# Kernel tuning notes

Measured on AMD Instinct MI355X. Metric: run time of the kernel, lower is better.

## Reference

```python
import jax, jax.numpy as jnp
import numpy as np

B, S, D_IN, D_K, D_OUT = 8, 2048, 1024, 64, 64

def setup_inputs() -> dict:
    key = jax.random.key(0)
    k1, k2, k3, k4 = jax.random.split(key, 4)
    sc = 1.0 / np.sqrt(D_IN)
    return {
        "X": jax.random.normal(k1, (B, S, D_IN), dtype=jnp.float32),
        "Wq": jax.random.normal(k2, (D_IN, D_K), dtype=jnp.float32) * sc,
        "Wk": jax.random.normal(k3, (D_IN, D_K), dtype=jnp.float32) * sc,
        "Wv": jax.random.normal(k4, (D_IN, D_OUT), dtype=jnp.float32) * sc,
    }

def reference(X, Wq, Wk, Wv):
    # projections (no bias)
    Q = jnp.einsum('bsd,dk->bsk', X, Wq)   # [B,S,d_k]
    K = jnp.einsum('bsd,dk->bsk', X, Wk)   # [B,S,d_k]
    V = jnp.einsum('bsd,dv->bsv', X, Wv)   # [B,S,d_out]
    d_k = Q.shape[-1]
    S_mat = jnp.einsum('bqk,bsk->bqs', Q, K) / jnp.sqrt(jnp.float32(d_k))
    # causal mask: positions j > i get -inf
    causal = jnp.tril(jnp.ones((X.shape[1], X.shape[1]), dtype=bool))
    S_mat = jnp.where(causal[None, :, :], S_mat, -jnp.inf)
    A = jax.nn.softmax(S_mat, axis=-1)
    return jnp.einsum('bqs,bsv->bqv', A, V)
```

## Files before the change

kernel.cpp:

```cpp
#include <hip/hip_runtime.h>
#include <hip/hip_bf16.h>
#include <cstdint>
#include <cstddef>

#define BATCH 8
#define SEQ   2048
#define DIN   1024

typedef float f32x4 __attribute__((ext_vector_type(4)));
typedef float f32x8 __attribute__((ext_vector_type(8)));
typedef __bf16 bf16x4 __attribute__((ext_vector_type(4)));
typedef __bf16 bf16x8 __attribute__((ext_vector_type(8)));
typedef unsigned short ushort8_t __attribute__((ext_vector_type(8)));

__device__ __forceinline__ unsigned short bfu(float f) {
  __bf16 h = (__bf16)f;
  return __builtin_bit_cast(unsigned short, h);
}

__device__ __forceinline__ bf16x8 cvt8pair(float4 a, float4 b) {
  f32x8 v;
  v[0] = a.x; v[1] = a.y; v[2] = a.z; v[3] = a.w;
  v[4] = b.x; v[5] = b.y; v[6] = b.z; v[7] = b.w;
  return __builtin_convertvector(v, bf16x8);
}

__global__ void pack_w(const float* __restrict__ Wq, const float* __restrict__ Wk,
                       const float* __restrict__ Wv, unsigned short* __restrict__ Wp) {
  const int t = blockIdx.x * blockDim.x + threadIdx.x;
  const int lane = t & 63;
  const int grp = t >> 6;
  const int ks = grp & 31;
  const int nt = grp >> 5;
  const int n = nt * 16 + (lane & 15);
  const int k0 = ks * 32 + ((lane >> 4) << 3);
  const float* W;
  int col;
  float scale = 1.0f;
  if (n < 64)       { W = Wq; col = n;       scale = 0.18033688011112042f; }
  else if (n < 128) { W = Wk; col = n - 64;  }
  else              { W = Wv; col = n - 128; }
  ushort8_t out;
#pragma unroll
  for (int j = 0; j < 8; ++j)
    out[j] = bfu(W[(size_t)(k0 + j) * 64 + col] * scale);
  reinterpret_cast<ushort8_t*>(Wp)[t] = out;
}

__global__ __launch_bounds__(256, 2) void qkv_gemm(
    const float* __restrict__ X, const unsigned short* __restrict__ Wp,
    unsigned short* __restrict__ Qb, unsigned short* __restrict__ Kf,
    unsigned short* __restrict__ Vf) {
  __shared__ ushort8_t Af[2][2048];

  const int tid = threadIdx.x;
  const int lane = tid & 63;
  const int wave = tid >> 6;
  const int l15 = lane & 15;
  const int quad = lane >> 4;
  const int m0 = blockIdx.x * 32;
  const int nt0 = wave * 3;

  const int sr = tid >> 3;
  const int sk = tid & 7;
  const float* xrow = X + (size_t)(m0 + sr) * DIN;

  const ushort8_t* wp = reinterpret_cast<const ushort8_t*>(Wp) + nt0 * 2048 + lane;
  ushort8_t breg[2][3];
#pragma unroll
  for (int p = 0; p < 2; ++p)
#pragma unroll
    for (int nt = 0; nt < 3; ++nt) breg[p][nt] = wp[p * 64 + nt * 2048];

  f32x4 acc[2][3];
#pragma unroll
  for (int mt = 0; mt < 2; ++mt)
#pragma unroll
    for (int nt = 0; nt < 3; ++nt) acc[mt][nt] = (f32x4){0.f, 0.f, 0.f, 0.f};

  auto compute_half = [&](int ksbase, const ushort8_t* A) {
    ushort8_t a0 = A[quad * 32 + l15];
    ushort8_t a1 = A[quad * 32 + 16 + l15];
    for (int ksl = 0; ksl < 16; ++ksl) {
      const int ks = ksbase + ksl;
      const int p = ks & 1;
      bf16x8 af0 = __builtin_bit_cast(bf16x8, a0);
      bf16x8 af1 = __builtin_bit_cast(bf16x8, a1);
      bf16x8 b0 = __builtin_bit_cast(bf16x8, breg[p][0]);
      bf16x8 b1 = __builtin_bit_cast(bf16x8, breg[p][1]);
      bf16x8 b2 = __builtin_bit_cast(bf16x8, breg[p][2]);
      if (ksl < 15) {
        a0 = A[((ksl + 1) * 4 + quad) * 32 + l15];
        a1 = A[((ksl + 1) * 4 + quad) * 32 + 16 + l15];
      }
      if (ks < 30) {
#pragma unroll
        for (int nt = 0; nt < 3; ++nt)
          breg[p][nt] = wp[(ks + 2) * 64 + nt * 2048];
      }
      acc[0][0] = __builtin_amdgcn_mfma_f32_16x16x32_bf16(af0, b0, acc[0][0], 0, 0, 0);
      acc[0][1] = __builtin_amdgcn_mfma_f32_16x16x32_bf16(af0, b1, acc[0][1], 0, 0, 0);
      acc[0][2] = __builtin_amdgcn_mfma_f32_16x16x32_bf16(af0, b2, acc[0][2], 0, 0, 0);
      acc[1][0] = __builtin_amdgcn_mfma_f32_16x16x32_bf16(af1, b0, acc[1][0], 0, 0, 0);
      acc[1][1] = __builtin_amdgcn_mfma_f32_16x16x32_bf16(af1, b1, acc[1][1], 0, 0, 0);
      acc[1][2] = __builtin_amdgcn_mfma_f32_16x16x32_bf16(af1, b2, acc[1][2], 0, 0, 0);
    }
  };

  float4 xbuf[16];
#pragma unroll
  for (int p = 0; p < 2; ++p) {
    const float4* src = reinterpret_cast<const float4*>(xrow + (sk + p * 8) * 32);
#pragma unroll
    for (int i = 0; i < 8; ++i) xbuf[p * 8 + i] = src[i];
  }
#pragma unroll
  for (int p = 0; p < 2; ++p) {
    const int ksl = sk + p * 8;
#pragma unroll
    for (int q = 0; q < 4; ++q)
      Af[0][(ksl * 4 + q) * 32 + sr] =
          __builtin_bit_cast(ushort8_t, cvt8pair(xbuf[p * 8 + q * 2], xbuf[p * 8 + q * 2 + 1]));
  }
  __syncthreads();

#pragma unroll
  for (int p = 0; p < 2; ++p) {
    const float4* src = reinterpret_cast<const float4*>(xrow + (16 + sk + p * 8) * 32);
#pragma unroll
    for (int i = 0; i < 8; ++i) xbuf[p * 8 + i] = src[i];
  }

  compute_half(0, Af[0]);

#pragma unroll
  for (int p = 0; p < 2; ++p) {
    const int ksl = sk + p * 8;
#pragma unroll
    for (int q = 0; q < 4; ++q)
      Af[1][(ksl * 4 + q) * 32 + sr] =
          __builtin_bit_cast(ushort8_t, cvt8pair(xbuf[p * 8 + q * 2], xbuf[p * 8 + q * 2 + 1]));
  }
  __syncthreads();

  compute_half(16, Af[1]);

#pragma unroll
  for (int mt = 0; mt < 2; ++mt) {
    const int srow = m0 + mt * 16 + quad * 4;
    const int b = srow >> 11;
    const int s = srow & 2047;
#pragma unroll
    for (int nt = 0; nt < 3; ++nt) {
      const f32x4 a = acc[mt][nt];
      const int n = (nt0 + nt) * 16 + l15;
      if (n < 64) {
#pragma unroll
        for (int r = 0; r < 4; ++r)
          Qb[(size_t)(srow + r) * 64 + n] = bfu(a[r]);
      } else if (n < 128) {
        const int dk = n - 64;
        const int dh = dk >> 5, kq = (dk >> 3) & 3, kj = dk & 7;
        const int kt = s >> 6, hh = (s >> 4) & 3;
        unsigned short* kdst = Kf + (((size_t)(b * 32 + kt) * 8 + hh * 2 + dh) << 9)
                                  + (kq * 16 + quad * 4) * 8 + kj;
#pragma unroll
        for (int r = 0; r < 4; ++r) kdst[r * 8] = bfu(a[r]);
      } else {
        const int dv = n - 128;
        const int vnt = dv >> 4, vl = dv & 15;
        const int kt = s >> 6, vc = (s >> 5) & 1, vq = (s >> 3) & 3, j0 = s & 7;
        ushort4 t4;
        t4.x = bfu(a[0]); t4.y = bfu(a[1]);
        t4.z = bfu(a[2]); t4.w = bfu(a[3]);
        *reinterpret_cast<ushort4*>(Vf + (((size_t)(b * 32 + kt) * 8 + vc * 4 + vnt) << 9)
                                       + (vq * 16 + vl) * 8 + j0) = t4;
      }
    }
  }
}

__global__ __launch_bounds__(256, 2) void flash_kernel(
    const unsigned short* __restrict__ Qb, const unsigned short* __restrict__ Kf,
    const unsigned short* __restrict__ Vf, float* __restrict__ Out) {
  __shared__ float Olds[4][2][16][68];
  __shared__ float Llds[4][2][16];
  __shared__ __attribute__((aligned(16))) unsigned short Pf[4][2][2][512];

  const int tid = threadIdx.x;
  const int lane = tid & 63;
  const int wave = tid >> 6;
  const int l15 = lane & 15;
  const int quad = lane >> 4;

  const int g = blockIdx.x;
  const int batch = g & 7;
  const int jj = (g >> 3) & 31;
  const int qb = (g < 256) ? (63 - jj) : jj;
  const int q0 = qb * 32;
  const int n64 = (q0 + 95) >> 6;

  bf16x8 qf[2][2];
#pragma unroll
  for (int mt = 0; mt < 2; ++mt) {
    const ushort8_t* qp = reinterpret_cast<const ushort8_t*>(
        Qb + (size_t)(batch * SEQ + q0 + mt * 16 + l15) * 64);
    qf[mt][0] = __builtin_bit_cast(bf16x8, qp[quad]);
    qf[mt][1] = __builtin_bit_cast(bf16x8, qp[4 + quad]);
  }

  const ushort8_t* kfb = reinterpret_cast<const ushort8_t*>(Kf)
                         + (size_t)batch * 32 * 512 + lane;
  const ushort8_t* vfb = reinterpret_cast<const ushort8_t*>(Vf)
                         + (size_t)batch * 32 * 512 + lane;

  const int pbase = l15 * 8 + (quad >> 1) * 128 + (quad & 1) * 4;

  f32x4 o[2][4];
  float lacc[2];
#pragma unroll
  for (int mt = 0; mt < 2; ++mt) {
    lacc[mt] = 0.f;
#pragma unroll
    for (int i = 0; i < 4; ++i) o[mt][i] = (f32x4){0.f, 0.f, 0.f, 0.f};
  }

  ushort8_t kbuf[8];
  if (wave < n64) {
    const ushort8_t* kp = kfb + wave * 512;
#pragma unroll
    for (int i = 0; i < 8; ++i) kbuf[i] = kp[i * 64];
  }

  for (int kt = wave; kt < n64; kt += 4) {
    const int k0 = kt * 64;
    f32x4 s[2][4];
    __builtin_amdgcn_s_setprio(1);
#pragma unroll
    for (int h = 0; h < 4; ++h) {
      bf16x8 kf0 = __builtin_bit_cast(bf16x8, kbuf[h * 2]);
      bf16x8 kf1 = __builtin_bit_cast(bf16x8, kbuf[h * 2 + 1]);
#pragma unroll
      for (int mt = 0; mt < 2; ++mt) {
        f32x4 z = (f32x4){0.f, 0.f, 0.f, 0.f};
        z = __builtin_amdgcn_mfma_f32_16x16x32_bf16(kf0, qf[mt][0], z, 0, 0, 0);
        z = __builtin_amdgcn_mfma_f32_16x16x32_bf16(kf1, qf[mt][1], z, 0, 0, 0);
        s[mt][h] = z;
      }
    }
    __builtin_amdgcn_s_setprio(0);
    {
      const int nk = (kt + 4 < n64) ? kt + 4 : n64 - 1;
      const ushort8_t* kp = kfb + nk * 512;
#pragma unroll
      for (int i = 0; i < 8; ++i) kbuf[i] = kp[i * 64];
    }
    ushort8_t vbuf[8];
    {
      const ushort8_t* vp = vfb + kt * 512;
#pragma unroll
      for (int i = 0; i < 8; ++i) vbuf[i] = vp[i * 64];
    }
    if (kt == n64 - 1) {
#pragma unroll
      for (int mt = 0; mt < 2; ++mt) {
        const int row = q0 + mt * 16 + l15;
#pragma unroll
        for (int h = 0; h < 4; ++h) {
          const int colb = k0 + h * 16 + quad * 4;
#pragma unroll
          for (int r = 0; r < 4; ++r)
            if (colb + r > row) s[mt][h][r] = -INFINITY;
        }
      }
    }
#pragma unroll
    for (int mt = 0; mt < 2; ++mt) {
#pragma unroll
      for (int h = 0; h < 4; ++h) {
        f32x4 p;
#pragma unroll
        for (int r = 0; r < 4; ++r) p[r] = __builtin_amdgcn_exp2f(s[mt][h][r]);
        lacc[mt] += (p[0] + p[1]) + (p[2] + p[3]);
        bf16x4 pk = __builtin_convertvector(p, bf16x4);
        *reinterpret_cast<unsigned long long*>(
            &Pf[wave][mt][h >> 1][pbase + ((h & 1) << 8)]) =
            __builtin_bit_cast(unsigned long long, pk);
      }
    }
#pragma unroll
    for (int c = 0; c < 2; ++c) {
      bf16x8 pfm[2];
#pragma unroll
      for (int mt = 0; mt < 2; ++mt)
        pfm[mt] = __builtin_bit_cast(bf16x8,
            reinterpret_cast<const ushort8_t*>(&Pf[wave][mt][c][0])[lane]);
      __builtin_amdgcn_s_setprio(1);
#pragma unroll
      for (int nt = 0; nt < 4; ++nt) {
        bf16x8 vf = __builtin_bit_cast(bf16x8, vbuf[c * 4 + nt]);
#pragma unroll
        for (int mt = 0; mt < 2; ++mt)
          o[mt][nt] = __builtin_amdgcn_mfma_f32_16x16x32_bf16(pfm[mt], vf, o[mt][nt], 0, 0, 0);
      }
      __builtin_amdgcn_s_setprio(0);
    }
  }

#pragma unroll
  for (int off = 16; off < 64; off <<= 1)
#pragma unroll
    for (int mt = 0; mt < 2; ++mt)
      lacc[mt] += __shfl_xor(lacc[mt], off, 64);

#pragma unroll
  for (int mt = 0; mt < 2; ++mt) {
#pragma unroll
    for (int nt = 0; nt < 4; ++nt)
#pragma unroll
      for (int r = 0; r < 4; ++r)
        Olds[wave][mt][quad * 4 + r][nt * 16 + l15] = o[mt][nt][r];
    if (quad == 0) Llds[wave][mt][l15] = lacc[mt];
  }
  __syncthreads();

  const int col = tid & 63;
  const int r0 = tid >> 6;
#pragma unroll
  for (int row = r0; row < 32; row += 4) {
    const int mt = row >> 4;
    const int rr = row & 15;
    float lstar = 0.f, accv = 0.f;
#pragma unroll
    for (int w = 0; w < 4; ++w) {
      lstar += Llds[w][mt][rr];
      accv += Olds[w][mt][rr][col];
    }
    Out[(size_t)(batch * SEQ + q0 + row) * 64 + col] = accv / lstar;
  }
}

extern "C" void kernel_launch(void* const* d_in, const int* in_sizes, int n_in,
                              void* d_out, int out_size, void* d_ws, size_t ws_size,
                              hipStream_t stream) {
  const float* X  = (const float*)d_in[0];
  const float* Wq = (const float*)d_in[1];
  const float* Wk = (const float*)d_in[2];
  const float* Wv = (const float*)d_in[3];
  float* Out = (float*)d_out;

  char* ws = (char*)d_ws;
  unsigned short* Wp = (unsigned short*)ws;
  unsigned short* Qb = (unsigned short*)(ws + (400 << 10));
  unsigned short* Kf = (unsigned short*)(ws + (400 << 10) + (2 << 20));
  unsigned short* Vf = (unsigned short*)(ws + (400 << 10) + (4 << 20));

  pack_w<<<96, 256, 0, stream>>>(Wq, Wk, Wv, Wp);
  qkv_gemm<<<512, 256, 0, stream>>>(X, Wp, Qb, Kf, Vf);
  flash_kernel<<<512, 256, 0, stream>>>(Qb, Kf, Vf, Out);
}
```

Before: 121.1 us.

## Use 64-row query tiles with 8 waves splitting KV tiles per block

The flash kernel now gives each block 64 query rows and 512 threads (8 waves), each wave handling every eighth KV tile, so each K/V tile load feeds four 16-row MMA groups instead of two. The grid halves to 256 blocks, and the reversed/paired query-block ordering used for causal load balancing is dropped. The cross-wave output reduction reuses the P scratch buffer in LDS one 16-row slice at a time, with extra barriers. This raises per-wave register pressure and leaves blocks with very uneven work because of the causal mask. Short query blocks also leave most waves idle.

```diff
diff --git a/kernel.cpp b/kernel.cpp
--- a/kernel.cpp
+++ b/kernel.cpp
@@ -180,12 +180,12 @@
   }
 }
 
-__global__ __launch_bounds__(256, 2) void flash_kernel(
+__global__ __launch_bounds__(512, 2) void flash_kernel(
     const unsigned short* __restrict__ Qb, const unsigned short* __restrict__ Kf,
     const unsigned short* __restrict__ Vf, float* __restrict__ Out) {
-  __shared__ float Olds[4][2][16][68];
-  __shared__ float Llds[4][2][16];
-  __shared__ __attribute__((aligned(16))) unsigned short Pf[4][2][2][512];
+  __shared__ __attribute__((aligned(16))) unsigned short Pf[8][4][2][512];
+  __shared__ float Llds[8][4][16];
+  float* Om = reinterpret_cast<float*>(&Pf[0][0][0][0]);
 
   const int tid = threadIdx.x;
   const int lane = tid & 63;
@@ -195,14 +195,13 @@
 
   const int g = blockIdx.x;
   const int batch = g & 7;
-  const int jj = (g >> 3) & 31;
-  const int qb = (g < 256) ? (63 - jj) : jj;
-  const int q0 = qb * 32;
-  const int n64 = (q0 + 95) >> 6;
-
-  bf16x8 qf[2][2];
-#pragma unroll
-  for (int mt = 0; mt < 2; ++mt) {
+  const int qb = g >> 3;
+  const int q0 = qb * 64;
+  const int n64 = qb + 1;
+
+  bf16x8 qf[4][2];
+#pragma unroll
+  for (int mt = 0; mt < 4; ++mt) {
     const ushort8_t* qp = reinterpret_cast<const ushort8_t*>(
         Qb + (size_t)(batch * SEQ + q0 + mt * 16 + l15) * 64);
     qf[mt][0] = __builtin_bit_cast(bf16x8, qp[quad]);
@@ -216,127 +215,127 @@
 
   const int pbase = l15 * 8 + (quad >> 1) * 128 + (quad & 1) * 4;
 
-  f32x4 o[2][4];
-  float lacc[2];
-#pragma unroll
-  for (int mt = 0; mt < 2; ++mt) {
+  f32x4 o[4][4];
+  float lacc[4];
+#pragma unroll
+  for (int mt = 0; mt < 4; ++mt) {
     lacc[mt] = 0.f;
 #pragma unroll
     for (int i = 0; i < 4; ++i) o[mt][i] = (f32x4){0.f, 0.f, 0.f, 0.f};
   }
 
-  ushort8_t kbuf[8];
+  ushort8_t kbuf[8], vbuf[8];
+
   if (wave < n64) {
-    const ushort8_t* kp = kfb + wave * 512;
-#pragma unroll
-    for (int i = 0; i < 8; ++i) kbuf[i] = kp[i * 64];
-  }
-
-  for (int kt = wave; kt < n64; kt += 4) {
-    const int k0 = kt * 64;
-    f32x4 s[2][4];
-    __builtin_amdgcn_s_setprio(1);
-#pragma unroll
-    for (int h = 0; h < 4; ++h) {
-      bf16x8 kf0 = __builtin_bit_cast(bf16x8, kbuf[h * 2]);
-      bf16x8 kf1 = __builtin_bit_cast(bf16x8, kbuf[h * 2 + 1]);
-#pragma unroll
-      for (int mt = 0; mt < 2; ++mt) {
-        f32x4 z = (f32x4){0.f, 0.f, 0.f, 0.f};
-        z = __builtin_amdgcn_mfma_f32_16x16x32_bf16(kf0, qf[mt][0], z, 0, 0, 0);
-        z = __builtin_amdgcn_mfma_f32_16x16x32_bf16(kf1, qf[mt][1], z, 0, 0, 0);
-        s[mt][h] = z;
-      }
-    }
-    __builtin_amdgcn_s_setprio(0);
     {
-      const int nk = (kt + 4 < n64) ? kt + 4 : n64 - 1;
-      const ushort8_t* kp = kfb + nk * 512;
+      const ushort8_t* kp = kfb + wave * 512;
 #pragma unroll
       for (int i = 0; i < 8; ++i) kbuf[i] = kp[i * 64];
     }
-    ushort8_t vbuf[8];
-    {
-      const ushort8_t* vp = vfb + kt * 512;
-#pragma unroll
-      for (int i = 0; i < 8; ++i) vbuf[i] = vp[i * 64];
-    }
-    if (kt == n64 - 1) {
-#pragma unroll
-      for (int mt = 0; mt < 2; ++mt) {
-        const int row = q0 + mt * 16 + l15;
+    for (int kt = wave; kt < n64; kt += 8) {
+      const int k0 = kt * 64;
+      const int nk = (kt + 8 < n64) ? kt + 8 : n64 - 1;
+      const bool diag = (kt == n64 - 1);
+#pragma unroll
+      for (int mt = 0; mt < 4; ++mt) {
+        f32x4 s[4];
+        __builtin_amdgcn_s_setprio(1);
 #pragma unroll
         for (int h = 0; h < 4; ++h) {
-          const int colb = k0 + h * 16 + quad * 4;
-#pragma unroll
-          for (int r = 0; r < 4; ++r)
-            if (colb + r > row) s[mt][h][r] = -INFINITY;
-        }
-      }
-    }
-#pragma unroll
-    for (int mt = 0; mt < 2; ++mt) {
-#pragma unroll
-      for (int h = 0; h < 4; ++h) {
-        f32x4 p;
-#pragma unroll
-        for (int r = 0; r < 4; ++r) p[r] = __builtin_amdgcn_exp2f(s[mt][h][r]);
-        lacc[mt] += (p[0] + p[1]) + (p[2] + p[3]);
-        bf16x4 pk = __builtin_convertvector(p, bf16x4);
-        *reinterpret_cast<unsigned long long*>(
-            &Pf[wave][mt][h >> 1][pbase + ((h & 1) << 8)]) =
-            __builtin_bit_cast(unsigned long long, pk);
-      }
-    }
-#pragma unroll
-    for (int c = 0; c < 2; ++c) {
-      bf16x8 pfm[2];
-#pragma unroll
-      for (int mt = 0; mt < 2; ++mt)
-        pfm[mt] = __builtin_bit_cast(bf16x8,
-            reinterpret_cast<const ushort8_t*>(&Pf[wave][mt][c][0])[lane]);
-      __builtin_amdgcn_s_setprio(1);
-#pragma unroll
-      for (int nt = 0; nt < 4; ++nt) {
-        bf16x8 vf = __builtin_bit_cast(bf16x8, vbuf[c * 4 + nt]);
-#pragma unroll
-        for (int mt = 0; mt < 2; ++mt)
-          o[mt][nt] = __builtin_amdgcn_mfma_f32_16x16x32_bf16(pfm[mt], vf, o[mt][nt], 0, 0, 0);
-      }
-      __builtin_amdgcn_s_setprio(0);
+          bf16x8 kf0 = __builtin_bit_cast(bf16x8, kbuf[h * 2]);
+          bf16x8 kf1 = __builtin_bit_cast(bf16x8, kbuf[h * 2 + 1]);
+          f32x4 z = (f32x4){0.f, 0.f, 0.f, 0.f};
+          z = __builtin_amdgcn_mfma_f32_16x16x32_bf16(kf0, qf[mt][0], z, 0, 0, 0);
+          z = __builtin_amdgcn_mfma_f32_16x16x32_bf16(kf1, qf[mt][1], z, 0, 0, 0);
+          s[h] = z;
+        }
+        __builtin_amdgcn_s_setprio(0);
+        if (diag) {
+          const int row = q0 + mt * 16 + l15;
+#pragma unroll
+          for (int h = 0; h < 4; ++h) {
+            const int colb = k0 + h * 16 + quad * 4;
+#pragma unroll
+            for (int r = 0; r < 4; ++r)
+              if (colb + r > row) s[h][r] = -INFINITY;
+          }
+        }
+#pragma unroll
+        for (int h = 0; h < 4; ++h) {
+          f32x4 p;
+#pragma unroll
+          for (int r = 0; r < 4; ++r) p[r] = __builtin_amdgcn_exp2f(s[h][r]);
+          lacc[mt] += (p[0] + p[1]) + (p[2] + p[3]);
+          *reinterpret_cast<unsigned long long*>(
+              &Pf[wave][mt][h >> 1][pbase + ((h & 1) << 8)]) =
+              __builtin_bit_cast(unsigned long long,
+                                 __builtin_convertvector(p, bf16x4));
+        }
+        if (mt == 1) {
+          const ushort8_t* vp = vfb + kt * 512;
+#pragma unroll
+          for (int i = 0; i < 8; ++i) vbuf[i] = vp[i * 64];
+        }
+      }
+      {
+        const ushort8_t* kp = kfb + nk * 512;
+#pragma unroll
+        for (int i = 0; i < 8; ++i) kbuf[i] = kp[i * 64];
+      }
+#pragma unroll
+      for (int c = 0; c < 2; ++c) {
+        bf16x8 pfm[4];
+#pragma unroll
+        for (int mt = 0; mt < 4; ++mt)
+          pfm[mt] = __builtin_bit_cast(bf16x8,
+              reinterpret_cast<const ushort8_t*>(&Pf[wave][mt][c][0])[lane]);
+        __builtin_amdgcn_s_setprio(1);
+#pragma unroll
+        for (int nt = 0; nt < 4; ++nt) {
+          bf16x8 vf = __builtin_bit_cast(bf16x8, vbuf[c * 4 + nt]);
+#pragma unroll
+          for (int mt = 0; mt < 4; ++mt)
+            o[mt][nt] = __builtin_amdgcn_mfma_f32_16x16x32_bf16(pfm[mt], vf, o[mt][nt], 0, 0, 0);
+        }
+        __builtin_amdgcn_s_setprio(0);
+      }
     }
   }
 
 #pragma unroll
   for (int off = 16; off < 64; off <<= 1)
 #pragma unroll
-    for (int mt = 0; mt < 2; ++mt)
+    for (int mt = 0; mt < 4; ++mt)
       lacc[mt] += __shfl_xor(lacc[mt], off, 64);
 
-#pragma unroll
-  for (int mt = 0; mt < 2; ++mt) {
+  if (quad == 0) {
+#pragma unroll
+    for (int mt = 0; mt < 4; ++mt) Llds[wave][mt][l15] = lacc[mt];
+  }
+  __syncthreads();
+
+  const int mcol = tid & 63;
+  const int mrow0 = tid >> 6;
+#pragma unroll
+  for (int mt = 0; mt < 4; ++mt) {
 #pragma unroll
     for (int nt = 0; nt < 4; ++nt)
 #pragma unroll
       for (int r = 0; r < 4; ++r)
-        Olds[wave][mt][quad * 4 + r][nt * 16 + l15] = o[mt][nt][r];
-    if (quad == 0) Llds[wave][mt][l15] = lacc[mt];
-  }
-  __syncthreads();
-
-  const int col = tid & 63;
-  const int r0 = tid >> 6;
-#pragma unroll
-  for (int row = r0; row < 32; row += 4) {
-    const int mt = row >> 4;
-    const int rr = row & 15;
-    float lstar = 0.f, accv = 0.f;
-#pragma unroll
-    for (int w = 0; w < 4; ++w) {
-      lstar += Llds[w][mt][rr];
-      accv += Olds[w][mt][rr][col];
-    }
-    Out[(size_t)(batch * SEQ + q0 + row) * 64 + col] = accv / lstar;
+        Om[(wave * 16 + quad * 4 + r) * 68 + nt * 16 + l15] = o[mt][nt][r];
+    __syncthreads();
+#pragma unroll
+    for (int half = 0; half < 2; ++half) {
+      const int row = mrow0 + half * 8;
+      float lstar = 0.f, accv = 0.f;
+#pragma unroll
+      for (int w = 0; w < 8; ++w) {
+        lstar += Llds[w][mt][row];
+        accv += Om[(w * 16 + row) * 68 + mcol];
+      }
+      Out[(size_t)(batch * SEQ + q0 + mt * 16 + row) * 64 + mcol] = accv / lstar;
+    }
+    __syncthreads();
   }
 }
 
@@ -357,5 +356,5 @@
 
   pack_w<<<96, 256, 0, stream>>>(Wq, Wk, Wv, Wp);
   qkv_gemm<<<512, 256, 0, stream>>>(X, Wp, Qb, Kf, Vf);
-  flash_kernel<<<512, 256, 0, stream>>>(Qb, Kf, Vf, Out);
-}
+  flash_kernel<<<256, 512, 0, stream>>>(Qb, Kf, Vf, Out);
+}
```

Measured after the change: 127.1 us. 4.9% more time.
